# Kernel tuning notes

Measured on AMD Instinct MI355X. Metric: run time of the kernel, lower is better.

The kernel has to match this reference:

```python
import jax, jax.numpy as jnp
import numpy as np

H = 3  # hidden size (matches nn.LSTM(3, 3, ...))


def _lstm_dir(x, Wih, Whh, bih, bhh, reverse):
    """One direction of one LSTM layer. x: [B,T,D]; PyTorch gate order i,f,g,o."""
    B = x.shape[0]
    xT = jnp.swapaxes(x, 0, 1)  # [T,B,D]
    # Precompute input projection for all timesteps (memory-bound GEMM once).
    x_proj = jnp.einsum('tbd,gd->tbg', xT, Wih) + (bih + bhh)  # [T,B,4H]

    def step(carry, xp):
        h, c = carry
        gates = xp + h @ Whh.T  # [B,4H]
        i = jax.nn.sigmoid(gates[:, :H])
        f = jax.nn.sigmoid(gates[:, H:2 * H])
        g = jnp.tanh(gates[:, 2 * H:3 * H])
        o = jax.nn.sigmoid(gates[:, 3 * H:])
        c = f * c + i * g
        h = o * jnp.tanh(c)
        return (h, c), h

    init = (jnp.zeros((B, H), x.dtype), jnp.zeros((B, H), x.dtype))
    _, hs = jax.lax.scan(step, init, x_proj, reverse=reverse)
    return jnp.swapaxes(hs, 0, 1)  # [B,T,H], time-aligned with input


def setup_inputs() -> dict:
    key = jax.random.key(0)
    ks = jax.random.split(key, 20)
    B, T = 8192, 512
    k = 1.0 / np.sqrt(H)

    def u(kk, shape):
        return jax.random.uniform(kk, shape, jnp.float32, -k, k)

    inp = {"x": jax.random.normal(ks[0], (B, T, 3), jnp.float32)}
    # layer 0: input dim 3; layer 1: input dim 2*H = 6
    inp.update({
        "W_ih_l0": u(ks[1], (4 * H, 3)),  "W_hh_l0": u(ks[2], (4 * H, H)),
        "b_ih_l0": u(ks[3], (4 * H,)),    "b_hh_l0": u(ks[4], (4 * H,)),
        "W_ih_l0r": u(ks[5], (4 * H, 3)), "W_hh_l0r": u(ks[6], (4 * H, H)),
        "b_ih_l0r": u(ks[7], (4 * H,)),   "b_hh_l0r": u(ks[8], (4 * H,)),
        "W_ih_l1": u(ks[9], (4 * H, 2 * H)),  "W_hh_l1": u(ks[10], (4 * H, H)),
        "b_ih_l1": u(ks[11], (4 * H,)),       "b_hh_l1": u(ks[12], (4 * H,)),
        "W_ih_l1r": u(ks[13], (4 * H, 2 * H)),"W_hh_l1r": u(ks[14], (4 * H, H)),
        "b_ih_l1r": u(ks[15], (4 * H,)),      "b_hh_l1r": u(ks[16], (4 * H,)),
        "W_lin": u(ks[17], (1, 2 * H)),       "b_lin": u(ks[18], (1,)),
    })
    return inp


def reference(x, W_ih_l0, W_hh_l0, b_ih_l0, b_hh_l0,
              W_ih_l0r, W_hh_l0r, b_ih_l0r, b_hh_l0r,
              W_ih_l1, W_hh_l1, b_ih_l1, b_hh_l1,
              W_ih_l1r, W_hh_l1r, b_ih_l1r, b_hh_l1r,
              W_lin, b_lin):
    # layer 0 (bidirectional)
    y0 = jnp.concatenate([
        _lstm_dir(x, W_ih_l0, W_hh_l0, b_ih_l0, b_hh_l0, False),
        _lstm_dir(x, W_ih_l0r, W_hh_l0r, b_ih_l0r, b_hh_l0r, True),
    ], axis=-1)  # [B,T,6]
    # layer 1 (bidirectional)
    y1 = jnp.concatenate([
        _lstm_dir(y0, W_ih_l1, W_hh_l1, b_ih_l1, b_hh_l1, False),
        _lstm_dir(y0, W_ih_l1r, W_hh_l1r, b_ih_l1r, b_hh_l1r, True),
    ], axis=-1)  # [B,T,6]
    last = y1[:, -1, :]  # [B,6]  (output sequence at final timestep)
    out = last @ W_lin.T + b_lin  # [B,1]
    return jax.nn.sigmoid(out.reshape(-1))  # [B]
```

## Files before the change

kernel.cpp:

```cpp
#include <hip/hip_runtime.h>


#define B_ 8192
#define T_ 512
#define LOG2E 1.4426950408889634f

typedef float v2f __attribute__((ext_vector_type(2)));

__device__ __forceinline__ float rcp_(float x)  { return __builtin_amdgcn_rcpf(x); }
__device__ __forceinline__ float exp2_(float x) { return __builtin_amdgcn_exp2f(x); }
__device__ __forceinline__ float sigm_(float x) {
  return rcp_(1.0f + exp2_(-LOG2E * x));
}
__device__ __forceinline__ float tanh_(float x) {
  return 1.0f - 2.0f * rcp_(1.0f + exp2_(2.0f * LOG2E * x));
}
__device__ __forceinline__ v2f sp(float s) { return (v2f){s, s}; }
__device__ __forceinline__ v2f pkfma(v2f a, float b, v2f c) {
  return __builtin_elementwise_fma(a, sp(b), c);
}

template <int CTRL>
__device__ __forceinline__ float dppf(float v) {
  int s = __float_as_int(v);
  return __int_as_float(__builtin_amdgcn_update_dpp(s, s, CTRL, 0xF, 0xF, false));
}
#define QB0 0x00
#define QB1 0x55
#define QB2 0xAA
#define SHR4 0x114

__global__ __launch_bounds__(256, 1) void lstm_l0_bwd(
    const float* __restrict__ x,
    const float* __restrict__ Wih, const float* __restrict__ Whh,
    const float* __restrict__ bih, const float* __restrict__ bhh,
    float* __restrict__ y0b)
{
  int tid = blockIdx.x * 256 + threadIdx.x;
  int b = tid >> 2, jl = tid & 3;
  int j = (jl < 3) ? jl : 0;
  const int r0 = j, r1 = 3 + j, r2 = 6 + j, r3 = 9 + j;

  v2f wif0 = {Wih[r0*3+0], Wih[r1*3+0]}, wif1 = {Wih[r0*3+1], Wih[r1*3+1]},
      wif2 = {Wih[r0*3+2], Wih[r1*3+2]};
  v2f wif3 = {Whh[r0*3+0], Whh[r1*3+0]}, wif4 = {Whh[r0*3+1], Whh[r1*3+1]},
      wif5 = {Whh[r0*3+2], Whh[r1*3+2]};
  v2f wgo0 = {Wih[r2*3+0], Wih[r3*3+0]}, wgo1 = {Wih[r2*3+1], Wih[r3*3+1]},
      wgo2 = {Wih[r2*3+2], Wih[r3*3+2]};
  v2f wgo3 = {Whh[r2*3+0], Whh[r3*3+0]}, wgo4 = {Whh[r2*3+1], Whh[r3*3+1]},
      wgo5 = {Whh[r2*3+2], Whh[r3*3+2]};
  v2f bif = {bih[r0]+bhh[r0], bih[r1]+bhh[r1]};
  v2f bgo = {bih[r2]+bhh[r2], bih[r3]+bhh[r3]};

  float h = 0.f, c = 0.f, hb0 = 0.f, hb1 = 0.f, hb2 = 0.f;
  const float4* xq = (const float4*)(x + (size_t)b * (T_ * 3));
  float* ywb = y0b + (size_t)b * (T_ * 3) + jl * 8;

  float hs0 = 0.f, hs1 = 0.f, hs2 = 0.f, hs3 = 0.f,
        hs4 = 0.f, hs5 = 0.f, hs6 = 0.f, hs7 = 0.f, h511 = 0.f;
  float4 p0, p1, p2, p3, p4, p5, q0, q1, q2, q3, q4, q5;

#define LD1(blk, r0_, r1_, r2_, r3_, r4_, r5_) do {                       \
    const float4* _p = xq + (blk) * 6;                                    \
    r0_ = _p[0]; r1_ = _p[1]; r2_ = _p[2];                                \
    r3_ = _p[3]; r4_ = _p[4]; r5_ = _p[5];                                \
    __builtin_amdgcn_sched_barrier(0); } while (0)

#define STEP1(x0, x1, x2, HOUT) do {                                      \
    v2f aif = pkfma(wif0, (x0), bif); aif = pkfma(wif1, (x1), aif);       \
    aif = pkfma(wif2, (x2), aif);                                         \
    v2f uif = wif3 * sp(hb0); uif = pkfma(wif4, hb1, uif);                \
    uif = pkfma(wif5, hb2, uif);                                          \
    v2f pif = aif + uif;                                                  \
    v2f ago = pkfma(wgo0, (x0), bgo); ago = pkfma(wgo1, (x1), ago);       \
    ago = pkfma(wgo2, (x2), ago);                                         \
    v2f ugo = wgo3 * sp(hb0); ugo = pkfma(wgo4, hb1, ugo);                \
    ugo = pkfma(wgo5, hb2, ugo);                                          \
    v2f pgo = ago + ugo;                                                  \
    v2f eif = pif * sp(-LOG2E);                                           \
    v2f ego = pgo * (v2f){2.f * LOG2E, -LOG2E};                           \
    float ig = rcp_(1.f + exp2_(eif.x));                                  \
    float fg = rcp_(1.f + exp2_(eif.y));                                  \
    float gg = 1.f - 2.f * rcp_(1.f + exp2_(ego.x));                      \
    float og = rcp_(1.f + exp2_(ego.y));                                  \
    c = fg * c + ig * gg;                                                 \
    h = og * tanh_(c);                                                    \
    hb0 = dppf<QB0>(h); hb1 = dppf<QB1>(h); hb2 = dppf<QB2>(h);           \
    HOUT = h; } while (0)

#define FLUSH1(yblk) do {                                                 \
    if (jl < 3) {                                                         \
      float4* _o = (float4*)(ywb + (yblk) * 24);                          \
      _o[0] = make_float4(hs0, hs1, hs2, hs3);                            \
      _o[1] = make_float4(hs4, hs5, hs6, hs7);                            \
    } } while (0)

#define PROC1(blk, r0_, r1_, r2_, r3_, r4_, r5_, FIRST) do {              \
    STEP1(r5_.y, r5_.z, r5_.w, hs0);                                      \
    if (FIRST) h511 = hs0; else FLUSH1((blk) + 1);                        \
    STEP1(r4_.z, r4_.w, r5_.x, hs7);                                      \
    STEP1(r3_.w, r4_.x, r4_.y, hs6);                                      \
    STEP1(r3_.x, r3_.y, r3_.z, hs5);                                      \
    STEP1(r2_.y, r2_.z, r2_.w, hs4);                                      \
    STEP1(r1_.z, r1_.w, r2_.x, hs3);                                      \
    STEP1(r0_.w, r1_.x, r1_.y, hs2);                                      \
    STEP1(r0_.x, r0_.y, r0_.z, hs1); } while (0)

  LD1(63, p0, p1, p2, p3, p4, p5);
  LD1(62, q0, q1, q2, q3, q4, q5);
  PROC1(63, p0, p1, p2, p3, p4, p5, true);
  LD1(61, p0, p1, p2, p3, p4, p5);
  PROC1(62, q0, q1, q2, q3, q4, q5, false);
  LD1(60, q0, q1, q2, q3, q4, q5);
  for (int blk = 61; blk >= 1; blk -= 2) {
    PROC1(blk, p0, p1, p2, p3, p4, p5, false);
    if (blk >= 3) LD1(blk - 2, p0, p1, p2, p3, p4, p5);
    PROC1(blk - 1, q0, q1, q2, q3, q4, q5, false);
    if (blk >= 3) LD1(blk - 3, q0, q1, q2, q3, q4, q5);
  }
  hs0 = h511;
  FLUSH1(0);
#undef LD1
#undef STEP1
#undef FLUSH1
#undef PROC1
}

__global__ __launch_bounds__(256, 1) void lstm_fused_fwd(
    const float* __restrict__ x,
    const float* __restrict__ Wih0, const float* __restrict__ Whh0,
    const float* __restrict__ bih0, const float* __restrict__ bhh0,
    const float* __restrict__ Wih1, const float* __restrict__ Whh1,
    const float* __restrict__ bih1, const float* __restrict__ bhh1,
    const float* __restrict__ Wih1r, const float* __restrict__ Whh1r,
    const float* __restrict__ bih1r, const float* __restrict__ bhh1r,
    const float* __restrict__ Wlin, const float* __restrict__ blin,
    const float* __restrict__ y0b,
    float* __restrict__ out)
{
  int tid = blockIdx.x * 256 + threadIdx.x;
  int b = tid >> 3, lane = tid & 7;
  bool role1 = lane >= 4;
  int j  = role1 ? (lane - 4) : lane;
  int jc = (j < 3) ? j : 2;
  const int r0 = jc, r1 = 3 + jc, r2 = 6 + jc, r3 = 9 + jc;

  v2f wif0, wif1, wif2, wif3, wif4, wif5, wif6, wif7, wif8;
  v2f wgo0, wgo1, wgo2, wgo3, wgo4, wgo5, wgo6, wgo7, wgo8;
  v2f bif, bgo;
  if (!role1) {
    wif0 = (v2f){Wih0[r0*3+0], Wih0[r1*3+0]};
    wif1 = (v2f){Wih0[r0*3+1], Wih0[r1*3+1]};
    wif2 = (v2f){Wih0[r0*3+2], Wih0[r1*3+2]};
    wif3 = (v2f){0.f, 0.f}; wif4 = (v2f){0.f, 0.f}; wif5 = (v2f){0.f, 0.f};
    wif6 = (v2f){Whh0[r0*3+0], Whh0[r1*3+0]};
    wif7 = (v2f){Whh0[r0*3+1], Whh0[r1*3+1]};
    wif8 = (v2f){Whh0[r0*3+2], Whh0[r1*3+2]};
    wgo0 = (v2f){Wih0[r2*3+0], Wih0[r3*3+0]};
    wgo1 = (v2f){Wih0[r2*3+1], Wih0[r3*3+1]};
    wgo2 = (v2f){Wih0[r2*3+2], Wih0[r3*3+2]};
    wgo3 = (v2f){0.f, 0.f}; wgo4 = (v2f){0.f, 0.f}; wgo5 = (v2f){0.f, 0.f};
    wgo6 = (v2f){Whh0[r2*3+0], Whh0[r3*3+0]};
    wgo7 = (v2f){Whh0[r2*3+1], Whh0[r3*3+1]};
    wgo8 = (v2f){Whh0[r2*3+2], Whh0[r3*3+2]};
    bif = (v2f){bih0[r0]+bhh0[r0], bih0[r1]+bhh0[r1]};
    bgo = (v2f){bih0[r2]+bhh0[r2], bih0[r3]+bhh0[r3]};
  } else {
    wif0 = (v2f){Wih1[r0*6+0], Wih1[r1*6+0]};
    wif1 = (v2f){Wih1[r0*6+1], Wih1[r1*6+1]};
    wif2 = (v2f){Wih1[r0*6+2], Wih1[r1*6+2]};
    wif3 = (v2f){Wih1[r0*6+3], Wih1[r1*6+3]};
    wif4 = (v2f){Wih1[r0*6+4], Wih1[r1*6+4]};
    wif5 = (v2f){Wih1[r0*6+5], Wih1[r1*6+5]};
    wif6 = (v2f){Whh1[r0*3+0], Whh1[r1*3+0]};
    wif7 = (v2f){Whh1[r0*3+1], Whh1[r1*3+1]};
    wif8 = (v2f){Whh1[r0*3+2], Whh1[r1*3+2]};
    wgo0 = (v2f){Wih1[r2*6+0], Wih1[r3*6+0]};
    wgo1 = (v2f){Wih1[r2*6+1], Wih1[r3*6+1]};
    wgo2 = (v2f){Wih1[r2*6+2], Wih1[r3*6+2]};
    wgo3 = (v2f){Wih1[r2*6+3], Wih1[r3*6+3]};
    wgo4 = (v2f){Wih1[r2*6+4], Wih1[r3*6+4]};
    wgo5 = (v2f){Wih1[r2*6+5], Wih1[r3*6+5]};
    wgo6 = (v2f){Whh1[r2*3+0], Whh1[r3*3+0]};
    wgo7 = (v2f){Whh1[r2*3+1], Whh1[r3*3+1]};
    wgo8 = (v2f){Whh1[r2*3+2], Whh1[r3*3+2]};
    bif = (v2f){bih1[r0]+bhh1[r0], bih1[r1]+bhh1[r1]};
    bgo = (v2f){bih1[r2]+bhh1[r2], bih1[r3]+bhh1[r3]};
  }

  float h = 0.f, c = 0.f;
  float ha0 = 0.f, ha1 = 0.f, ha2 = 0.f;
  float hb0 = 0.f, hb1 = 0.f, hb2 = 0.f;
  const float4* baseq =
      (const float4*)((role1 ? y0b : x) + (size_t)b * (T_ * 3));

  const float* up = y0b + (size_t)b * (T_ * 3);
  float ub0 = up[0], ub1 = up[8], ub2 = up[16];

  float4 p0, p1, p2, p3, p4, p5, q0, q1, q2, q3, q4, q5;

#define LD2(blk, r0_, r1_, r2_, r3_, r4_, r5_) do {                       \
    const float4* _p = baseq + (blk) * 6;                                 \
    r0_ = _p[0]; r1_ = _p[1]; r2_ = _p[2];                                \
    r3_ = _p[3]; r4_ = _p[4]; r5_ = _p[5];                                \
    __builtin_amdgcn_sched_barrier(0); } while (0)

#define GATES2(m0, m1, m2, n0, n1, n2)                     \
    float v0 = role1 ? hb0 : (m0);                                        \
    float v1 = role1 ? hb1 : (m1);                                        \
    float v2 = role1 ? hb2 : (m2);                                        \
    v2f aif = pkfma(wif0, v0, bif); aif = pkfma(wif1, v1, aif);           \
    aif = pkfma(wif2, v2, aif);                                           \
    aif = pkfma(wif3, (n0), aif); aif = pkfma(wif4, (n1), aif);           \
    v2f uif = wif5 * sp(n2); uif = pkfma(wif6, ha0, uif);                 \
    uif = pkfma(wif7, ha1, uif); uif = pkfma(wif8, ha2, uif);             \
    v2f pif = aif + uif;                                                  \
    v2f ago = pkfma(wgo0, v0, bgo); ago = pkfma(wgo1, v1, ago);           \
    ago = pkfma(wgo2, v2, ago);                                           \
    ago = pkfma(wgo3, (n0), ago); ago = pkfma(wgo4, (n1), ago);           \
    v2f ugo = wgo5 * sp(n2); ugo = pkfma(wgo6, ha0, ugo);                 \
    ugo = pkfma(wgo7, ha1, ugo); ugo = pkfma(wgo8, ha2, ugo);             \
    v2f pgo = ago + ugo;                                                  \
    v2f eif = pif * sp(-LOG2E);                                           \
    v2f ego = pgo * (v2f){2.f * LOG2E, -LOG2E};                           \
    float ig = rcp_(1.f + exp2_(eif.x));                                  \
    float fg = rcp_(1.f + exp2_(eif.y));                                  \
    float gg = 1.f - 2.f * rcp_(1.f + exp2_(ego.x));                      \
    float og = rcp_(1.f + exp2_(ego.y));                                  \
    float cn = fg * c + ig * gg;                                          \
    float hn = og * tanh_(cn);

#define BCAST2() do {                                                     \
    ha0 = dppf<QB0>(h); ha1 = dppf<QB1>(h); ha2 = dppf<QB2>(h);           \
    hb0 = dppf<SHR4>(ha0); hb1 = dppf<SHR4>(ha1); hb2 = dppf<SHR4>(ha2);  \
  } while (0)

#define STEP2(m0, m1, m2, n0, n1, n2) do {                                \
    GATES2(m0, m1, m2, n0, n1, n2)                                        \
    c = cn; h = hn;                                                       \
    BCAST2(); } while (0)

#define STEP2V(m0, m1, m2, n0, n1, n2, VALID) do {                        \
    GATES2(m0, m1, m2, n0, n1, n2)                                        \
    c = (VALID) ? cn : c; h = (VALID) ? hn : h;                           \
    BCAST2(); } while (0)

#define PROC2(r0_, r1_, r2_, r3_, r4_, r5_) do {                          \
    STEP2(r0_.x, r0_.y, r0_.z,  r0_.x, r2_.x, r4_.x);                     \
    STEP2(r0_.w, r1_.x, r1_.y,  r0_.y, r2_.y, r4_.y);                     \
    STEP2(r1_.z, r1_.w, r2_.x,  r0_.z, r2_.z, r4_.z);                     \
    STEP2(r2_.y, r2_.z, r2_.w,  r0_.w, r2_.w, r4_.w);                     \
    STEP2(r3_.x, r3_.y, r3_.z,  r1_.x, r3_.x, r5_.x);                     \
    STEP2(r3_.w, r4_.x, r4_.y,  r1_.y, r3_.y, r5_.y);                     \
    STEP2(r4_.z, r4_.w, r5_.x,  r1_.z, r3_.z, r5_.z);                     \
    STEP2(r5_.y, r5_.z, r5_.w,  r1_.w, r3_.w, r5_.w); } while (0)

  LD2(0, p0, p1, p2, p3, p4, p5);
  LD2(1, q0, q1, q2, q3, q4, q5);
  STEP2V(p0.x, p0.y, p0.z,  p0.x, p2.x, p4.x, !role1);
  STEP2(p0.w, p1.x, p1.y,  p0.y, p2.y, p4.y);
  STEP2(p1.z, p1.w, p2.x,  p0.z, p2.z, p4.z);
  STEP2(p2.y, p2.z, p2.w,  p0.w, p2.w, p4.w);
  STEP2(p3.x, p3.y, p3.z,  p1.x, p3.x, p5.x);
  STEP2(p3.w, p4.x, p4.y,  p1.y, p3.y, p5.y);
  STEP2(p4.z, p4.w, p5.x,  p1.z, p3.z, p5.z);
  STEP2(p5.y, p5.z, p5.w,  p1.w, p3.w, p5.w);
  LD2(2, p0, p1, p2, p3, p4, p5);
  PROC2(q0, q1, q2, q3, q4, q5);
  LD2(3, q0, q1, q2, q3, q4, q5);
  for (int blk = 2; blk < 64; blk += 2) {
    PROC2(p0, p1, p2, p3, p4, p5);
    if (blk + 2 < 64) LD2(blk + 2, p0, p1, p2, p3, p4, p5);
    PROC2(q0, q1, q2, q3, q4, q5);
    if (blk + 3 < 64) LD2(blk + 3, q0, q1, q2, q3, q4, q5);
  }
  STEP2V(ub0, ub1, ub2,  ub0, ub1, ub2, role1);

  float e0 = role1 ? hb0 : ha0;
  float e1 = role1 ? hb1 : ha1;
  float e2 = role1 ? hb2 : ha2;

  float h1b;
  {
    float q_i = bih1r[r0] + bhh1r[r0]
              + Wih1r[r0*6+0]*e0 + Wih1r[r0*6+1]*e1 + Wih1r[r0*6+2]*e2
              + Wih1r[r0*6+3]*ub0 + Wih1r[r0*6+4]*ub1 + Wih1r[r0*6+5]*ub2;
    float q_g = bih1r[r2] + bhh1r[r2]
              + Wih1r[r2*6+0]*e0 + Wih1r[r2*6+1]*e1 + Wih1r[r2*6+2]*e2
              + Wih1r[r2*6+3]*ub0 + Wih1r[r2*6+4]*ub1 + Wih1r[r2*6+5]*ub2;
    float q_o = bih1r[r3] + bhh1r[r3]
              + Wih1r[r3*6+0]*e0 + Wih1r[r3*6+1]*e1 + Wih1r[r3*6+2]*e2
              + Wih1r[r3*6+3]*ub0 + Wih1r[r3*6+4]*ub1 + Wih1r[r3*6+5]*ub2;
    float ig = sigm_(q_i), gg = tanh_(q_g), og = sigm_(q_o);
    h1b = og * tanh_(ig * gg);
  }

  float part = 0.f;
  if (role1) { if (j < 3) part = Wlin[j]     * h;   }
  else       { if (j < 3) part = Wlin[3 + j] * h1b; }
  part += __shfl_xor(part, 1, 8);
  part += __shfl_xor(part, 2, 8);
  part += __shfl_xor(part, 4, 8);
  if (lane == 0) out[b] = sigm_(part + blin[0]);
#undef LD2
#undef GATES2
#undef BCAST2
#undef STEP2
#undef STEP2V
#undef PROC2
}

extern "C" void kernel_launch(void* const* d_in, const int* in_sizes, int n_in,
                              void* d_out, int out_size, void* d_ws, size_t ws_size,
                              hipStream_t stream) {
  const float* x        = (const float*)d_in[0];
  const float* W_ih_l0  = (const float*)d_in[1];
  const float* W_hh_l0  = (const float*)d_in[2];
  const float* b_ih_l0  = (const float*)d_in[3];
  const float* b_hh_l0  = (const float*)d_in[4];
  const float* W_ih_l0r = (const float*)d_in[5];
  const float* W_hh_l0r = (const float*)d_in[6];
  const float* b_ih_l0r = (const float*)d_in[7];
  const float* b_hh_l0r = (const float*)d_in[8];
  const float* W_ih_l1  = (const float*)d_in[9];
  const float* W_hh_l1  = (const float*)d_in[10];
  const float* b_ih_l1  = (const float*)d_in[11];
  const float* b_hh_l1  = (const float*)d_in[12];
  const float* W_ih_l1r = (const float*)d_in[13];
  const float* W_hh_l1r = (const float*)d_in[14];
  const float* b_ih_l1r = (const float*)d_in[15];
  const float* b_hh_l1r = (const float*)d_in[16];
  const float* W_lin    = (const float*)d_in[17];
  const float* b_lin    = (const float*)d_in[18];

  float* y0b = (float*)d_ws;
  float* out = (float*)d_out;

  lstm_l0_bwd<<<(B_ * 4) / 256, 256, 0, stream>>>(
      x, W_ih_l0r, W_hh_l0r, b_ih_l0r, b_hh_l0r, y0b);

  lstm_fused_fwd<<<(B_ * 8) / 256, 256, 0, stream>>>(
      x, W_ih_l0, W_hh_l0, b_ih_l0, b_hh_l0,
      W_ih_l1, W_hh_l1, b_ih_l1, b_hh_l1,
      W_ih_l1r, W_hh_l1r, b_ih_l1r, b_hh_l1r,
      W_lin, b_lin, y0b, out);
}
```

Baseline: 151.9 us.

## Split gate pairs across lanes to double thread parallelism per LSTM cell

Each hidden unit's four gates were computed by one lane as two packed pairs. They are now split across two lanes: one computes i/f, the other g/o, and the results are exchanged with DPP row shifts. Thread counts double for both kernels, and launch bounds move to two blocks per CU. This halves the per-lane transcendental and FMA work on the serial recurrence chain and adds parallelism, at the cost of extra DPP shuffles and selects per step and more redundant input loads.

```diff
diff --git a/kernel.cpp b/kernel.cpp
--- a/kernel.cpp
+++ b/kernel.cpp
@@ -28,33 +28,34 @@
 #define QB0 0x00
 #define QB1 0x55
 #define QB2 0xAA
+#define SHL4 0x104
 #define SHR4 0x114
-
-__global__ __launch_bounds__(256, 1) void lstm_l0_bwd(
+#define SHR8 0x118
+
+__global__ __launch_bounds__(256, 2) void lstm_l0_bwd(
     const float* __restrict__ x,
     const float* __restrict__ Wih, const float* __restrict__ Whh,
     const float* __restrict__ bih, const float* __restrict__ bhh,
     float* __restrict__ y0b)
 {
   int tid = blockIdx.x * 256 + threadIdx.x;
-  int b = tid >> 2, jl = tid & 3;
-  int j = (jl < 3) ? jl : 0;
-  const int r0 = j, r1 = 3 + j, r2 = 6 + j, r3 = 9 + j;
-
-  v2f wif0 = {Wih[r0*3+0], Wih[r1*3+0]}, wif1 = {Wih[r0*3+1], Wih[r1*3+1]},
-      wif2 = {Wih[r0*3+2], Wih[r1*3+2]};
-  v2f wif3 = {Whh[r0*3+0], Whh[r1*3+0]}, wif4 = {Whh[r0*3+1], Whh[r1*3+1]},
-      wif5 = {Whh[r0*3+2], Whh[r1*3+2]};
-  v2f wgo0 = {Wih[r2*3+0], Wih[r3*3+0]}, wgo1 = {Wih[r2*3+1], Wih[r3*3+1]},
-      wgo2 = {Wih[r2*3+2], Wih[r3*3+2]};
-  v2f wgo3 = {Whh[r2*3+0], Whh[r3*3+0]}, wgo4 = {Whh[r2*3+1], Whh[r3*3+1]},
-      wgo5 = {Whh[r2*3+2], Whh[r3*3+2]};
-  v2f bif = {bih[r0]+bhh[r0], bih[r1]+bhh[r1]};
-  v2f bgo = {bih[r2]+bhh[r2], bih[r3]+bhh[r3]};
-
-  float h = 0.f, c = 0.f, hb0 = 0.f, hb1 = 0.f, hb2 = 0.f;
+  int b = tid >> 3, lane = tid & 7;
+  bool qgo = (lane & 4) != 0;
+  int j = lane & 3; int jj = (j < 3) ? j : 0;
+  const int ra = (qgo ? 6 : 0) + jj, rb = ra + 3;
+
+  v2f w0 = {Wih[ra*3+0], Wih[rb*3+0]}, w1 = {Wih[ra*3+1], Wih[rb*3+1]},
+      w2 = {Wih[ra*3+2], Wih[rb*3+2]};
+  v2f u0 = {Whh[ra*3+0], Whh[rb*3+0]}, u1 = {Whh[ra*3+1], Whh[rb*3+1]},
+      u2 = {Whh[ra*3+2], Whh[rb*3+2]};
+  v2f b2 = {bih[ra]+bhh[ra], bih[rb]+bhh[rb]};
+  v2f sv = qgo ? (v2f){-2.f*LOG2E, -LOG2E} : (v2f){-LOG2E, -LOG2E};
+  v2f av = qgo ? (v2f){2.f, 1.f}  : (v2f){1.f, 1.f};
+  v2f dv = qgo ? (v2f){-1.f, 0.f} : (v2f){0.f, 0.f};
+
+  float h = 0.f, c = 0.f, ha0 = 0.f, ha1 = 0.f, ha2 = 0.f;
   const float4* xq = (const float4*)(x + (size_t)b * (T_ * 3));
-  float* ywb = y0b + (size_t)b * (T_ * 3) + jl * 8;
+  float* ywb = y0b + (size_t)b * (T_ * 3) + jj * 8;
 
   float hs0 = 0.f, hs1 = 0.f, hs2 = 0.f, hs3 = 0.f,
         hs4 = 0.f, hs5 = 0.f, hs6 = 0.f, hs7 = 0.f, h511 = 0.f;
@@ -67,29 +68,29 @@
     __builtin_amdgcn_sched_barrier(0); } while (0)
 
 #define STEP1(x0, x1, x2, HOUT) do {                                      \
-    v2f aif = pkfma(wif0, (x0), bif); aif = pkfma(wif1, (x1), aif);       \
-    aif = pkfma(wif2, (x2), aif);                                         \
-    v2f uif = wif3 * sp(hb0); uif = pkfma(wif4, hb1, uif);                \
-    uif = pkfma(wif5, hb2, uif);                                          \
-    v2f pif = aif + uif;                                                  \
-    v2f ago = pkfma(wgo0, (x0), bgo); ago = pkfma(wgo1, (x1), ago);       \
-    ago = pkfma(wgo2, (x2), ago);                                         \
-    v2f ugo = wgo3 * sp(hb0); ugo = pkfma(wgo4, hb1, ugo);                \
-    ugo = pkfma(wgo5, hb2, ugo);                                          \
-    v2f pgo = ago + ugo;                                                  \
-    v2f eif = pif * sp(-LOG2E);                                           \
-    v2f ego = pgo * (v2f){2.f * LOG2E, -LOG2E};                           \
-    float ig = rcp_(1.f + exp2_(eif.x));                                  \
-    float fg = rcp_(1.f + exp2_(eif.y));                                  \
-    float gg = 1.f - 2.f * rcp_(1.f + exp2_(ego.x));                      \
-    float og = rcp_(1.f + exp2_(ego.y));                                  \
-    c = fg * c + ig * gg;                                                 \
-    h = og * tanh_(c);                                                    \
-    hb0 = dppf<QB0>(h); hb1 = dppf<QB1>(h); hb2 = dppf<QB2>(h);           \
+    v2f pv = pkfma(w0, (x0), b2); pv = pkfma(w1, (x1), pv);               \
+    pv = pkfma(w2, (x2), pv);                                             \
+    v2f uv = u0 * sp(ha0); uv = pkfma(u1, ha1, uv);                       \
+    uv = pkfma(u2, ha2, uv);                                              \
+    pv = pv + uv;                                                         \
+    v2f e = pv * sv;                                                      \
+    float r0v = rcp_(1.f + exp2_(e.x));                                   \
+    float r1v = rcp_(1.f + exp2_(e.y));                                   \
+    float axv = __builtin_fmaf(av.x, r0v, dv.x);                          \
+    float ayv = __builtin_fmaf(av.y, r1v, dv.y);                          \
+    float slx = dppf<SHL4>(axv), sly = dppf<SHL4>(ayv);                   \
+    float srx = dppf<SHR4>(axv), sry = dppf<SHR4>(ayv);                   \
+    float gi = qgo ? srx : axv;                                           \
+    float gf = qgo ? sry : ayv;                                           \
+    float gG = qgo ? axv : slx;                                           \
+    float gO = qgo ? ayv : sly;                                           \
+    c = gf * c + gi * gG;                                                 \
+    h = gO * tanh_(c);                                                    \
+    ha0 = dppf<QB0>(h); ha1 = dppf<QB1>(h); ha2 = dppf<QB2>(h);           \
     HOUT = h; } while (0)
 
 #define FLUSH1(yblk) do {                                                 \
-    if (jl < 3) {                                                         \
+    if (lane < 3) {                                                       \
       float4* _o = (float4*)(ywb + (yblk) * 24);                          \
       _o[0] = make_float4(hs0, hs1, hs2, hs3);                            \
       _o[1] = make_float4(hs4, hs5, hs6, hs7);                            \
@@ -126,7 +127,7 @@
 #undef PROC1
 }
 
-__global__ __launch_bounds__(256, 1) void lstm_fused_fwd(
+__global__ __launch_bounds__(256, 2) void lstm_fused_fwd(
     const float* __restrict__ x,
     const float* __restrict__ Wih0, const float* __restrict__ Whh0,
     const float* __restrict__ bih0, const float* __restrict__ bhh0,
@@ -139,60 +140,43 @@
     float* __restrict__ out)
 {
   int tid = blockIdx.x * 256 + threadIdx.x;
-  int b = tid >> 3, lane = tid & 7;
-  bool role1 = lane >= 4;
-  int j  = role1 ? (lane - 4) : lane;
-  int jc = (j < 3) ? j : 2;
-  const int r0 = jc, r1 = 3 + jc, r2 = 6 + jc, r3 = 9 + jc;
-
-  v2f wif0, wif1, wif2, wif3, wif4, wif5, wif6, wif7, wif8;
-  v2f wgo0, wgo1, wgo2, wgo3, wgo4, wgo5, wgo6, wgo7, wgo8;
-  v2f bif, bgo;
-  if (!role1) {
-    wif0 = (v2f){Wih0[r0*3+0], Wih0[r1*3+0]};
-    wif1 = (v2f){Wih0[r0*3+1], Wih0[r1*3+1]};
-    wif2 = (v2f){Wih0[r0*3+2], Wih0[r1*3+2]};
-    wif3 = (v2f){0.f, 0.f}; wif4 = (v2f){0.f, 0.f}; wif5 = (v2f){0.f, 0.f};
-    wif6 = (v2f){Whh0[r0*3+0], Whh0[r1*3+0]};
-    wif7 = (v2f){Whh0[r0*3+1], Whh0[r1*3+1]};
-    wif8 = (v2f){Whh0[r0*3+2], Whh0[r1*3+2]};
-    wgo0 = (v2f){Wih0[r2*3+0], Wih0[r3*3+0]};
-    wgo1 = (v2f){Wih0[r2*3+1], Wih0[r3*3+1]};
-    wgo2 = (v2f){Wih0[r2*3+2], Wih0[r3*3+2]};
-    wgo3 = (v2f){0.f, 0.f}; wgo4 = (v2f){0.f, 0.f}; wgo5 = (v2f){0.f, 0.f};
-    wgo6 = (v2f){Whh0[r2*3+0], Whh0[r3*3+0]};
-    wgo7 = (v2f){Whh0[r2*3+1], Whh0[r3*3+1]};
-    wgo8 = (v2f){Whh0[r2*3+2], Whh0[r3*3+2]};
-    bif = (v2f){bih0[r0]+bhh0[r0], bih0[r1]+bhh0[r1]};
-    bgo = (v2f){bih0[r2]+bhh0[r2], bih0[r3]+bhh0[r3]};
+  int b = tid >> 4, lane = tid & 15;
+  bool cell1 = lane >= 8;
+  bool qgo = (lane & 4) != 0;
+  int j = lane & 3; int jj = (j < 3) ? j : 0;
+  const int ra = (qgo ? 6 : 0) + jj, rb = ra + 3;
+
+  v2f w0, w1, w2, w3, w4, w5, u0, u1, u2, b2;
+  if (!cell1) {
+    w0 = (v2f){Wih0[ra*3+0], Wih0[rb*3+0]};
+    w1 = (v2f){Wih0[ra*3+1], Wih0[rb*3+1]};
+    w2 = (v2f){Wih0[ra*3+2], Wih0[rb*3+2]};
+    w3 = (v2f){0.f, 0.f}; w4 = (v2f){0.f, 0.f}; w5 = (v2f){0.f, 0.f};
+    u0 = (v2f){Whh0[ra*3+0], Whh0[rb*3+0]};
+    u1 = (v2f){Whh0[ra*3+1], Whh0[rb*3+1]};
+    u2 = (v2f){Whh0[ra*3+2], Whh0[rb*3+2]};
+    b2 = (v2f){bih0[ra]+bhh0[ra], bih0[rb]+bhh0[rb]};
   } else {
-    wif0 = (v2f){Wih1[r0*6+0], Wih1[r1*6+0]};
-    wif1 = (v2f){Wih1[r0*6+1], Wih1[r1*6+1]};
-    wif2 = (v2f){Wih1[r0*6+2], Wih1[r1*6+2]};
-    wif3 = (v2f){Wih1[r0*6+3], Wih1[r1*6+3]};
-    wif4 = (v2f){Wih1[r0*6+4], Wih1[r1*6+4]};
-    wif5 = (v2f){Wih1[r0*6+5], Wih1[r1*6+5]};
-    wif6 = (v2f){Whh1[r0*3+0], Whh1[r1*3+0]};
-    wif7 = (v2f){Whh1[r0*3+1], Whh1[r1*3+1]};
-    wif8 = (v2f){Whh1[r0*3+2], Whh1[r1*3+2]};
-    wgo0 = (v2f){Wih1[r2*6+0], Wih1[r3*6+0]};
-    wgo1 = (v2f){Wih1[r2*6+1], Wih1[r3*6+1]};
-    wgo2 = (v2f){Wih1[r2*6+2], Wih1[r3*6+2]};
-    wgo3 = (v2f){Wih1[r2*6+3], Wih1[r3*6+3]};
-    wgo4 = (v2f){Wih1[r2*6+4], Wih1[r3*6+4]};
-    wgo5 = (v2f){Wih1[r2*6+5], Wih1[r3*6+5]};
-    wgo6 = (v2f){Whh1[r2*3+0], Whh1[r3*3+0]};
-    wgo7 = (v2f){Whh1[r2*3+1], Whh1[r3*3+1]};
-    wgo8 = (v2f){Whh1[r2*3+2], Whh1[r3*3+2]};
-    bif = (v2f){bih1[r0]+bhh1[r0], bih1[r1]+bhh1[r1]};
-    bgo = (v2f){bih1[r2]+bhh1[r2], bih1[r3]+bhh1[r3]};
+    w0 = (v2f){Wih1[ra*6+0], Wih1[rb*6+0]};
+    w1 = (v2f){Wih1[ra*6+1], Wih1[rb*6+1]};
+    w2 = (v2f){Wih1[ra*6+2], Wih1[rb*6+2]};
+    w3 = (v2f){Wih1[ra*6+3], Wih1[rb*6+3]};
+    w4 = (v2f){Wih1[ra*6+4], Wih1[rb*6+4]};
+    w5 = (v2f){Wih1[ra*6+5], Wih1[rb*6+5]};
+    u0 = (v2f){Whh1[ra*3+0], Whh1[rb*3+0]};
+    u1 = (v2f){Whh1[ra*3+1], Whh1[rb*3+1]};
+    u2 = (v2f){Whh1[ra*3+2], Whh1[rb*3+2]};
+    b2 = (v2f){bih1[ra]+bhh1[ra], bih1[rb]+bhh1[rb]};
   }
+  v2f sv = qgo ? (v2f){-2.f*LOG2E, -LOG2E} : (v2f){-LOG2E, -LOG2E};
+  v2f av = qgo ? (v2f){2.f, 1.f}  : (v2f){1.f, 1.f};
+  v2f dv = qgo ? (v2f){-1.f, 0.f} : (v2f){0.f, 0.f};
 
   float h = 0.f, c = 0.f;
   float ha0 = 0.f, ha1 = 0.f, ha2 = 0.f;
   float hb0 = 0.f, hb1 = 0.f, hb2 = 0.f;
   const float4* baseq =
-      (const float4*)((role1 ? y0b : x) + (size_t)b * (T_ * 3));
+      (const float4*)((cell1 ? y0b : x) + (size_t)b * (T_ * 3));
 
   const float* up = y0b + (size_t)b * (T_ * 3);
   float ub0 = up[0], ub1 = up[8], ub2 = up[16];
@@ -206,33 +190,32 @@
     __builtin_amdgcn_sched_barrier(0); } while (0)
 
 #define GATES2(m0, m1, m2, n0, n1, n2)                     \
-    float v0 = role1 ? hb0 : (m0);                                        \
-    float v1 = role1 ? hb1 : (m1);                                        \
-    float v2 = role1 ? hb2 : (m2);                                        \
-    v2f aif = pkfma(wif0, v0, bif); aif = pkfma(wif1, v1, aif);           \
-    aif = pkfma(wif2, v2, aif);                                           \
-    aif = pkfma(wif3, (n0), aif); aif = pkfma(wif4, (n1), aif);           \
-    v2f uif = wif5 * sp(n2); uif = pkfma(wif6, ha0, uif);                 \
-    uif = pkfma(wif7, ha1, uif); uif = pkfma(wif8, ha2, uif);             \
-    v2f pif = aif + uif;                                                  \
-    v2f ago = pkfma(wgo0, v0, bgo); ago = pkfma(wgo1, v1, ago);           \
-    ago = pkfma(wgo2, v2, ago);                                           \
-    ago = pkfma(wgo3, (n0), ago); ago = pkfma(wgo4, (n1), ago);           \
-    v2f ugo = wgo5 * sp(n2); ugo = pkfma(wgo6, ha0, ugo);                 \
-    ugo = pkfma(wgo7, ha1, ugo); ugo = pkfma(wgo8, ha2, ugo);             \
-    v2f pgo = ago + ugo;                                                  \
-    v2f eif = pif * sp(-LOG2E);                                           \
-    v2f ego = pgo * (v2f){2.f * LOG2E, -LOG2E};                           \
-    float ig = rcp_(1.f + exp2_(eif.x));                                  \
-    float fg = rcp_(1.f + exp2_(eif.y));                                  \
-    float gg = 1.f - 2.f * rcp_(1.f + exp2_(ego.x));                      \
-    float og = rcp_(1.f + exp2_(ego.y));                                  \
-    float cn = fg * c + ig * gg;                                          \
-    float hn = og * tanh_(cn);
+    float i0 = cell1 ? hb0 : (m0);                                        \
+    float i1 = cell1 ? hb1 : (m1);                                        \
+    float i2 = cell1 ? hb2 : (m2);                                        \
+    v2f pv = pkfma(w0, i0, b2); pv = pkfma(w1, i1, pv);                   \
+    pv = pkfma(w2, i2, pv);                                               \
+    pv = pkfma(w3, (n0), pv); pv = pkfma(w4, (n1), pv);                   \
+    v2f uv = w5 * sp(n2); uv = pkfma(u0, ha0, uv);                        \
+    uv = pkfma(u1, ha1, uv); uv = pkfma(u2, ha2, uv);                     \
+    pv = pv + uv;                                                         \
+    v2f e = pv * sv;                                                      \
+    float r0v = rcp_(1.f + exp2_(e.x));                                   \
+    float r1v = rcp_(1.f + exp2_(e.y));                                   \
+    float axv = __builtin_fmaf(av.x, r0v, dv.x);                          \
+    float ayv = __builtin_fmaf(av.y, r1v, dv.y);                          \
+    float slx = dppf<SHL4>(axv), sly = dppf<SHL4>(ayv);                   \
+    float srx = dppf<SHR4>(axv), sry = dppf<SHR4>(ayv);                   \
+    float gi = qgo ? srx : axv;                                           \
+    float gf = qgo ? sry : ayv;                                           \
+    float gG = qgo ? axv : slx;                                           \
+    float gO = qgo ? ayv : sly;                                           \
+    float cn = gf * c + gi * gG;                                          \
+    float hn = gO * tanh_(cn);
 
 #define BCAST2() do {                                                     \
     ha0 = dppf<QB0>(h); ha1 = dppf<QB1>(h); ha2 = dppf<QB2>(h);           \
-    hb0 = dppf<SHR4>(ha0); hb1 = dppf<SHR4>(ha1); hb2 = dppf<SHR4>(ha2);  \
+    hb0 = dppf<SHR8>(ha0); hb1 = dppf<SHR8>(ha1); hb2 = dppf<SHR8>(ha2);  \
   } while (0)
 
 #define STEP2(m0, m1, m2, n0, n1, n2) do {                                \
@@ -257,7 +240,7 @@
 
   LD2(0, p0, p1, p2, p3, p4, p5);
   LD2(1, q0, q1, q2, q3, q4, q5);
-  STEP2V(p0.x, p0.y, p0.z,  p0.x, p2.x, p4.x, !role1);
+  STEP2V(p0.x, p0.y, p0.z,  p0.x, p2.x, p4.x, !cell1);
   STEP2(p0.w, p1.x, p1.y,  p0.y, p2.y, p4.y);
   STEP2(p1.z, p1.w, p2.x,  p0.z, p2.z, p4.z);
   STEP2(p2.y, p2.z, p2.w,  p0.w, p2.w, p4.w);
@@ -274,33 +257,45 @@
     PROC2(q0, q1, q2, q3, q4, q5);
     if (blk + 3 < 64) LD2(blk + 3, q0, q1, q2, q3, q4, q5);
   }
-  STEP2V(ub0, ub1, ub2,  ub0, ub1, ub2, role1);
-
-  float e0 = role1 ? hb0 : ha0;
-  float e1 = role1 ? hb1 : ha1;
-  float e2 = role1 ? hb2 : ha2;
+  STEP2V(ub0, ub1, ub2,  ub0, ub1, ub2, cell1);
+
+  float e0 = cell1 ? hb0 : ha0;
+  float e1 = cell1 ? hb1 : ha1;
+  float e2 = cell1 ? hb2 : ha2;
 
   float h1b;
   {
-    float q_i = bih1r[r0] + bhh1r[r0]
-              + Wih1r[r0*6+0]*e0 + Wih1r[r0*6+1]*e1 + Wih1r[r0*6+2]*e2
-              + Wih1r[r0*6+3]*ub0 + Wih1r[r0*6+4]*ub1 + Wih1r[r0*6+5]*ub2;
-    float q_g = bih1r[r2] + bhh1r[r2]
-              + Wih1r[r2*6+0]*e0 + Wih1r[r2*6+1]*e1 + Wih1r[r2*6+2]*e2
-              + Wih1r[r2*6+3]*ub0 + Wih1r[r2*6+4]*ub1 + Wih1r[r2*6+5]*ub2;
-    float q_o = bih1r[r3] + bhh1r[r3]
-              + Wih1r[r3*6+0]*e0 + Wih1r[r3*6+1]*e1 + Wih1r[r3*6+2]*e2
-              + Wih1r[r3*6+3]*ub0 + Wih1r[r3*6+4]*ub1 + Wih1r[r3*6+5]*ub2;
-    float ig = sigm_(q_i), gg = tanh_(q_g), og = sigm_(q_o);
-    h1b = og * tanh_(ig * gg);
+    v2f x0w = {Wih1r[ra*6+0], Wih1r[rb*6+0]};
+    v2f x1w = {Wih1r[ra*6+1], Wih1r[rb*6+1]};
+    v2f x2w = {Wih1r[ra*6+2], Wih1r[rb*6+2]};
+    v2f x3w = {Wih1r[ra*6+3], Wih1r[rb*6+3]};
+    v2f x4w = {Wih1r[ra*6+4], Wih1r[rb*6+4]};
+    v2f x5w = {Wih1r[ra*6+5], Wih1r[rb*6+5]};
+    v2f brv = {bih1r[ra]+bhh1r[ra], bih1r[rb]+bhh1r[rb]};
+    v2f pv = pkfma(x0w, e0, brv); pv = pkfma(x1w, e1, pv);
+    pv = pkfma(x2w, e2, pv);      pv = pkfma(x3w, ub0, pv);
+    pv = pkfma(x4w, ub1, pv);     pv = pkfma(x5w, ub2, pv);
+    v2f e = pv * sv;
+    float r0v = rcp_(1.f + exp2_(e.x));
+    float r1v = rcp_(1.f + exp2_(e.y));
+    float axv = __builtin_fmaf(av.x, r0v, dv.x);
+    float ayv = __builtin_fmaf(av.y, r1v, dv.y);
+    float slx = dppf<SHL4>(axv);
+    float sly = dppf<SHL4>(ayv);
+    float srx = dppf<SHR4>(axv);
+    float gi = qgo ? srx : axv;
+    float gG = qgo ? axv : slx;
+    float gO = qgo ? ayv : sly;
+    float cb = gi * gG;
+    h1b = gO * tanh_(cb);
   }
 
   float part = 0.f;
-  if (role1) { if (j < 3) part = Wlin[j]     * h;   }
-  else       { if (j < 3) part = Wlin[3 + j] * h1b; }
-  part += __shfl_xor(part, 1, 8);
-  part += __shfl_xor(part, 2, 8);
-  part += __shfl_xor(part, 4, 8);
+  if (!qgo && j < 3) part = cell1 ? (Wlin[j] * h) : (Wlin[3 + j] * h1b);
+  part += __shfl_xor(part, 1, 16);
+  part += __shfl_xor(part, 2, 16);
+  part += __shfl_xor(part, 4, 16);
+  part += __shfl_xor(part, 8, 16);
   if (lane == 0) out[b] = sigm_(part + blin[0]);
 #undef LD2
 #undef GATES2
@@ -336,10 +331,10 @@
   float* y0b = (float*)d_ws;
   float* out = (float*)d_out;
 
-  lstm_l0_bwd<<<(B_ * 4) / 256, 256, 0, stream>>>(
+  lstm_l0_bwd<<<(B_ * 8) / 256, 256, 0, stream>>>(
       x, W_ih_l0r, W_hh_l0r, b_ih_l0r, b_hh_l0r, y0b);
 
-  lstm_fused_fwd<<<(B_ * 8) / 256, 256, 0, stream>>>(
+  lstm_fused_fwd<<<(B_ * 16) / 256, 256, 0, stream>>>(
       x, W_ih_l0, W_hh_l0, b_ih_l0, b_hh_l0,
       W_ih_l1, W_hh_l1, b_ih_l1, b_hh_l1,
       W_ih_l1r, W_hh_l1r, b_ih_l1r, b_hh_l1r,
```

Result: slower. 189.9 us (+25.1%).

## Split backward layer-0 gates across 8 lanes and pre-scale weights by log2e

Applied to the files above, without the earlier changes.

The backward layer-0 kernel now uses 8 lanes per batch row instead of 4. Each half computes two gates (i/f or g/o), and partial products are exchanged with DPP row shifts, which halves the per-lane gate arithmetic on the serial recurrence. Weights and biases in both kernels are pre-multiplied by -log2e (or -2log2e for g) so the exp2 arguments need no extra scaling per step. The fused kernel also splits the accumulation chains into shorter parallel sums. The cost is twice as many threads and extra DPP and select instructions in each step.

```diff
diff --git a/kernel.cpp b/kernel.cpp
--- a/kernel.cpp
+++ b/kernel.cpp
@@ -15,6 +15,8 @@
 __device__ __forceinline__ float tanh_(float x) {
   return 1.0f - 2.0f * rcp_(1.0f + exp2_(2.0f * LOG2E * x));
 }
+__device__ __forceinline__ float act_(float p) { return rcp_(1.f + exp2_(p)); }
+
 __device__ __forceinline__ v2f sp(float s) { return (v2f){s, s}; }
 __device__ __forceinline__ v2f pkfma(v2f a, float b, v2f c) {
   return __builtin_elementwise_fma(a, sp(b), c);
@@ -28,6 +30,7 @@
 #define QB0 0x00
 #define QB1 0x55
 #define QB2 0xAA
+#define SHL4 0x104
 #define SHR4 0x114
 
 __global__ __launch_bounds__(256, 1) void lstm_l0_bwd(
@@ -37,24 +40,26 @@
     float* __restrict__ y0b)
 {
   int tid = blockIdx.x * 256 + threadIdx.x;
-  int b = tid >> 2, jl = tid & 3;
-  int j = (jl < 3) ? jl : 0;
-  const int r0 = j, r1 = 3 + j, r2 = 6 + j, r3 = 9 + j;
-
-  v2f wif0 = {Wih[r0*3+0], Wih[r1*3+0]}, wif1 = {Wih[r0*3+1], Wih[r1*3+1]},
-      wif2 = {Wih[r0*3+2], Wih[r1*3+2]};
-  v2f wif3 = {Whh[r0*3+0], Whh[r1*3+0]}, wif4 = {Whh[r0*3+1], Whh[r1*3+1]},
-      wif5 = {Whh[r0*3+2], Whh[r1*3+2]};
-  v2f wgo0 = {Wih[r2*3+0], Wih[r3*3+0]}, wgo1 = {Wih[r2*3+1], Wih[r3*3+1]},
-      wgo2 = {Wih[r2*3+2], Wih[r3*3+2]};
-  v2f wgo3 = {Whh[r2*3+0], Whh[r3*3+0]}, wgo4 = {Whh[r2*3+1], Whh[r3*3+1]},
-      wgo5 = {Whh[r2*3+2], Whh[r3*3+2]};
-  v2f bif = {bih[r0]+bhh[r0], bih[r1]+bhh[r1]};
-  v2f bgo = {bih[r2]+bhh[r2], bih[r3]+bhh[r3]};
-
-  float h = 0.f, c = 0.f, hb0 = 0.f, hb1 = 0.f, hb2 = 0.f;
+  int b = tid >> 3, lane = tid & 7;
+  bool qgo = (lane & 4) != 0;
+  int j = lane & 3; int jj = (j < 3) ? j : 0;
+  const int ra = (qgo ? 6 : 0) + jj, rb = ra + 3;
+  const float kx = qgo ? (-2.f * LOG2E) : (-LOG2E);
+  const float ky = -LOG2E;
+
+  v2f w0 = {Wih[ra*3+0]*kx, Wih[rb*3+0]*ky},
+      w1 = {Wih[ra*3+1]*kx, Wih[rb*3+1]*ky},
+      w2 = {Wih[ra*3+2]*kx, Wih[rb*3+2]*ky};
+  v2f u0 = {Whh[ra*3+0]*kx, Whh[rb*3+0]*ky},
+      u1 = {Whh[ra*3+1]*kx, Whh[rb*3+1]*ky},
+      u2 = {Whh[ra*3+2]*kx, Whh[rb*3+2]*ky};
+  v2f b2 = {(bih[ra]+bhh[ra])*kx, (bih[rb]+bhh[rb])*ky};
+  const float avx = qgo ? 2.f : 1.f;
+  const float dvx = qgo ? -1.f : 0.f;
+
+  float h = 0.f, c = 0.f, ha0 = 0.f, ha1 = 0.f, ha2 = 0.f;
   const float4* xq = (const float4*)(x + (size_t)b * (T_ * 3));
-  float* ywb = y0b + (size_t)b * (T_ * 3) + jl * 8;
+  float* ywb = y0b + (size_t)b * (T_ * 3) + jj * 8;
 
   float hs0 = 0.f, hs1 = 0.f, hs2 = 0.f, hs3 = 0.f,
         hs4 = 0.f, hs5 = 0.f, hs6 = 0.f, hs7 = 0.f, h511 = 0.f;
@@ -67,29 +72,28 @@
     __builtin_amdgcn_sched_barrier(0); } while (0)
 
 #define STEP1(x0, x1, x2, HOUT) do {                                      \
-    v2f aif = pkfma(wif0, (x0), bif); aif = pkfma(wif1, (x1), aif);       \
-    aif = pkfma(wif2, (x2), aif);                                         \
-    v2f uif = wif3 * sp(hb0); uif = pkfma(wif4, hb1, uif);                \
-    uif = pkfma(wif5, hb2, uif);                                          \
-    v2f pif = aif + uif;                                                  \
-    v2f ago = pkfma(wgo0, (x0), bgo); ago = pkfma(wgo1, (x1), ago);       \
-    ago = pkfma(wgo2, (x2), ago);                                         \
-    v2f ugo = wgo3 * sp(hb0); ugo = pkfma(wgo4, hb1, ugo);                \
-    ugo = pkfma(wgo5, hb2, ugo);                                          \
-    v2f pgo = ago + ugo;                                                  \
-    v2f eif = pif * sp(-LOG2E);                                           \
-    v2f ego = pgo * (v2f){2.f * LOG2E, -LOG2E};                           \
-    float ig = rcp_(1.f + exp2_(eif.x));                                  \
-    float fg = rcp_(1.f + exp2_(eif.y));                                  \
-    float gg = 1.f - 2.f * rcp_(1.f + exp2_(ego.x));                      \
-    float og = rcp_(1.f + exp2_(ego.y));                                  \
-    c = fg * c + ig * gg;                                                 \
-    h = og * tanh_(c);                                                    \
-    hb0 = dppf<QB0>(h); hb1 = dppf<QB1>(h); hb2 = dppf<QB2>(h);           \
+    v2f pv = pkfma(w0, (x0), b2); pv = pkfma(w1, (x1), pv);               \
+    pv = pkfma(w2, (x2), pv);                                             \
+    v2f uv = u0 * sp(ha0); uv = pkfma(u1, ha1, uv);                       \
+    uv = pkfma(u2, ha2, uv);                                              \
+    pv = pv + uv;                                                         \
+    float r0v = act_(pv.x);                                               \
+    float ayv = act_(pv.y);                         \
+    float axv = __builtin_fmaf(avx, r0v, dvx);  \
+    float slx = dppf<SHL4>(axv), sly = dppf<SHL4>(ayv);                   \
+    float srx = dppf<SHR4>(axv), sry = dppf<SHR4>(ayv);                   \
+    float pig = axv * (qgo ? srx : slx);           \
+    float gf  = qgo ? sry : ayv;                                          \
+    float gO  = qgo ? ayv : sly;                                          \
+    c = __builtin_fmaf(gf, c, pig);                                       \
+    float th = __builtin_fmaf(                                            \
+        2.f, rcp_(1.f + exp2_(-2.f * LOG2E * c)), -1.f);                  \
+    h = gO * th;                                                          \
+    ha0 = dppf<QB0>(h); ha1 = dppf<QB1>(h); ha2 = dppf<QB2>(h);           \
     HOUT = h; } while (0)
 
 #define FLUSH1(yblk) do {                                                 \
-    if (jl < 3) {                                                         \
+    if (lane < 3) {                                                       \
       float4* _o = (float4*)(ywb + (yblk) * 24);                          \
       _o[0] = make_float4(hs0, hs1, hs2, hs3);                            \
       _o[1] = make_float4(hs4, hs5, hs6, hs7);                            \
@@ -144,48 +148,49 @@
   int j  = role1 ? (lane - 4) : lane;
   int jc = (j < 3) ? j : 2;
   const int r0 = jc, r1 = 3 + jc, r2 = 6 + jc, r3 = 9 + jc;
+  const float sI = -LOG2E, sG = -2.f * LOG2E;
 
   v2f wif0, wif1, wif2, wif3, wif4, wif5, wif6, wif7, wif8;
   v2f wgo0, wgo1, wgo2, wgo3, wgo4, wgo5, wgo6, wgo7, wgo8;
   v2f bif, bgo;
   if (!role1) {
-    wif0 = (v2f){Wih0[r0*3+0], Wih0[r1*3+0]};
-    wif1 = (v2f){Wih0[r0*3+1], Wih0[r1*3+1]};
-    wif2 = (v2f){Wih0[r0*3+2], Wih0[r1*3+2]};
+    wif0 = (v2f){Wih0[r0*3+0]*sI, Wih0[r1*3+0]*sI};
+    wif1 = (v2f){Wih0[r0*3+1]*sI, Wih0[r1*3+1]*sI};
+    wif2 = (v2f){Wih0[r0*3+2]*sI, Wih0[r1*3+2]*sI};
     wif3 = (v2f){0.f, 0.f}; wif4 = (v2f){0.f, 0.f}; wif5 = (v2f){0.f, 0.f};
-    wif6 = (v2f){Whh0[r0*3+0], Whh0[r1*3+0]};
-    wif7 = (v2f){Whh0[r0*3+1], Whh0[r1*3+1]};
-    wif8 = (v2f){Whh0[r0*3+2], Whh0[r1*3+2]};
-    wgo0 = (v2f){Wih0[r2*3+0], Wih0[r3*3+0]};
-    wgo1 = (v2f){Wih0[r2*3+1], Wih0[r3*3+1]};
-    wgo2 = (v2f){Wih0[r2*3+2], Wih0[r3*3+2]};
+    wif6 = (v2f){Whh0[r0*3+0]*sI, Whh0[r1*3+0]*sI};
+    wif7 = (v2f){Whh0[r0*3+1]*sI, Whh0[r1*3+1]*sI};
+    wif8 = (v2f){Whh0[r0*3+2]*sI, Whh0[r1*3+2]*sI};
+    wgo0 = (v2f){Wih0[r2*3+0]*sG, Wih0[r3*3+0]*sI};
+    wgo1 = (v2f){Wih0[r2*3+1]*sG, Wih0[r3*3+1]*sI};
+    wgo2 = (v2f){Wih0[r2*3+2]*sG, Wih0[r3*3+2]*sI};
     wgo3 = (v2f){0.f, 0.f}; wgo4 = (v2f){0.f, 0.f}; wgo5 = (v2f){0.f, 0.f};
-    wgo6 = (v2f){Whh0[r2*3+0], Whh0[r3*3+0]};
-    wgo7 = (v2f){Whh0[r2*3+1], Whh0[r3*3+1]};
-    wgo8 = (v2f){Whh0[r2*3+2], Whh0[r3*3+2]};
-    bif = (v2f){bih0[r0]+bhh0[r0], bih0[r1]+bhh0[r1]};
-    bgo = (v2f){bih0[r2]+bhh0[r2], bih0[r3]+bhh0[r3]};
+    wgo6 = (v2f){Whh0[r2*3+0]*sG, Whh0[r3*3+0]*sI};
+    wgo7 = (v2f){Whh0[r2*3+1]*sG, Whh0[r3*3+1]*sI};
+    wgo8 = (v2f){Whh0[r2*3+2]*sG, Whh0[r3*3+2]*sI};
+    bif = (v2f){(bih0[r0]+bhh0[r0])*sI, (bih0[r1]+bhh0[r1])*sI};
+    bgo = (v2f){(bih0[r2]+bhh0[r2])*sG, (bih0[r3]+bhh0[r3])*sI};
   } else {
-    wif0 = (v2f){Wih1[r0*6+0], Wih1[r1*6+0]};
-    wif1 = (v2f){Wih1[r0*6+1], Wih1[r1*6+1]};
-    wif2 = (v2f){Wih1[r0*6+2], Wih1[r1*6+2]};
-    wif3 = (v2f){Wih1[r0*6+3], Wih1[r1*6+3]};
-    wif4 = (v2f){Wih1[r0*6+4], Wih1[r1*6+4]};
-    wif5 = (v2f){Wih1[r0*6+5], Wih1[r1*6+5]};
-    wif6 = (v2f){Whh1[r0*3+0], Whh1[r1*3+0]};
-    wif7 = (v2f){Whh1[r0*3+1], Whh1[r1*3+1]};
-    wif8 = (v2f){Whh1[r0*3+2], Whh1[r1*3+2]};
-    wgo0 = (v2f){Wih1[r2*6+0], Wih1[r3*6+0]};
-    wgo1 = (v2f){Wih1[r2*6+1], Wih1[r3*6+1]};
-    wgo2 = (v2f){Wih1[r2*6+2], Wih1[r3*6+2]};
-    wgo3 = (v2f){Wih1[r2*6+3], Wih1[r3*6+3]};
-    wgo4 = (v2f){Wih1[r2*6+4], Wih1[r3*6+4]};
-    wgo5 = (v2f){Wih1[r2*6+5], Wih1[r3*6+5]};
-    wgo6 = (v2f){Whh1[r2*3+0], Whh1[r3*3+0]};
-    wgo7 = (v2f){Whh1[r2*3+1], Whh1[r3*3+1]};
-    wgo8 = (v2f){Whh1[r2*3+2], Whh1[r3*3+2]};
-    bif = (v2f){bih1[r0]+bhh1[r0], bih1[r1]+bhh1[r1]};
-    bgo = (v2f){bih1[r2]+bhh1[r2], bih1[r3]+bhh1[r3]};
+    wif0 = (v2f){Wih1[r0*6+0]*sI, Wih1[r1*6+0]*sI};
+    wif1 = (v2f){Wih1[r0*6+1]*sI, Wih1[r1*6+1]*sI};
+    wif2 = (v2f){Wih1[r0*6+2]*sI, Wih1[r1*6+2]*sI};
+    wif3 = (v2f){Wih1[r0*6+3]*sI, Wih1[r1*6+3]*sI};
+    wif4 = (v2f){Wih1[r0*6+4]*sI, Wih1[r1*6+4]*sI};
+    wif5 = (v2f){Wih1[r0*6+5]*sI, Wih1[r1*6+5]*sI};
+    wif6 = (v2f){Whh1[r0*3+0]*sI, Whh1[r1*3+0]*sI};
+    wif7 = (v2f){Whh1[r0*3+1]*sI, Whh1[r1*3+1]*sI};
+    wif8 = (v2f){Whh1[r0*3+2]*sI, Whh1[r1*3+2]*sI};
+    wgo0 = (v2f){Wih1[r2*6+0]*sG, Wih1[r3*6+0]*sI};
+    wgo1 = (v2f){Wih1[r2*6+1]*sG, Wih1[r3*6+1]*sI};
+    wgo2 = (v2f){Wih1[r2*6+2]*sG, Wih1[r3*6+2]*sI};
+    wgo3 = (v2f){Wih1[r2*6+3]*sG, Wih1[r3*6+3]*sI};
+    wgo4 = (v2f){Wih1[r2*6+4]*sG, Wih1[r3*6+4]*sI};
+    wgo5 = (v2f){Wih1[r2*6+5]*sG, Wih1[r3*6+5]*sI};
+    wgo6 = (v2f){Whh1[r2*3+0]*sG, Whh1[r3*3+0]*sI};
+    wgo7 = (v2f){Whh1[r2*3+1]*sG, Whh1[r3*3+1]*sI};
+    wgo8 = (v2f){Whh1[r2*3+2]*sG, Whh1[r3*3+2]*sI};
+    bif = (v2f){(bih1[r0]+bhh1[r0])*sI, (bih1[r1]+bhh1[r1])*sI};
+    bgo = (v2f){(bih1[r2]+bhh1[r2])*sG, (bih1[r3]+bhh1[r3])*sI};
   }
 
   float h = 0.f, c = 0.f;
@@ -211,24 +216,26 @@
     float v2 = role1 ? hb2 : (m2);                                        \
     v2f aif = pkfma(wif0, v0, bif); aif = pkfma(wif1, v1, aif);           \
     aif = pkfma(wif2, v2, aif);                                           \
-    aif = pkfma(wif3, (n0), aif); aif = pkfma(wif4, (n1), aif);           \
-    v2f uif = wif5 * sp(n2); uif = pkfma(wif6, ha0, uif);                 \
-    uif = pkfma(wif7, ha1, uif); uif = pkfma(wif8, ha2, uif);             \
-    v2f pif = aif + uif;                                                  \
+    v2f nif = wif3 * sp(n0); nif = pkfma(wif4, (n1), nif);                \
+    nif = pkfma(wif5, (n2), nif);                                         \
+    v2f uif = wif6 * sp(ha0); uif = pkfma(wif7, ha1, uif);                \
+    uif = pkfma(wif8, ha2, uif);                                          \
+    v2f pif = (aif + nif) + uif;                                          \
     v2f ago = pkfma(wgo0, v0, bgo); ago = pkfma(wgo1, v1, ago);           \
     ago = pkfma(wgo2, v2, ago);                                           \
-    ago = pkfma(wgo3, (n0), ago); ago = pkfma(wgo4, (n1), ago);           \
-    v2f ugo = wgo5 * sp(n2); ugo = pkfma(wgo6, ha0, ugo);                 \
-    ugo = pkfma(wgo7, ha1, ugo); ugo = pkfma(wgo8, ha2, ugo);             \
-    v2f pgo = ago + ugo;                                                  \
-    v2f eif = pif * sp(-LOG2E);                                           \
-    v2f ego = pgo * (v2f){2.f * LOG2E, -LOG2E};                           \
-    float ig = rcp_(1.f + exp2_(eif.x));                                  \
-    float fg = rcp_(1.f + exp2_(eif.y));                                  \
-    float gg = 1.f - 2.f * rcp_(1.f + exp2_(ego.x));                      \
-    float og = rcp_(1.f + exp2_(ego.y));                                  \
-    float cn = fg * c + ig * gg;                                          \
-    float hn = og * tanh_(cn);
+    v2f ngo = wgo3 * sp(n0); ngo = pkfma(wgo4, (n1), ngo);                \
+    ngo = pkfma(wgo5, (n2), ngo);                                         \
+    v2f ugo = wgo6 * sp(ha0); ugo = pkfma(wgo7, ha1, ugo);                \
+    ugo = pkfma(wgo8, ha2, ugo);                                          \
+    v2f pgo = (ago + ngo) + ugo;                                          \
+    float ig = act_(pif.x);                                               \
+    float fg = act_(pif.y);                                               \
+    float gg = __builtin_fmaf(2.f, act_(pgo.x), -1.f);                    \
+    float og = act_(pgo.y);                                               \
+    float cn = __builtin_fmaf(fg, c, ig * gg);                            \
+    float th = __builtin_fmaf(                                            \
+        2.f, rcp_(1.f + exp2_(-2.f * LOG2E * cn)), -1.f);                 \
+    float hn = og * th;
 
 #define BCAST2() do {                                                     \
     ha0 = dppf<QB0>(h); ha1 = dppf<QB1>(h); ha2 = dppf<QB2>(h);           \
@@ -336,7 +343,7 @@
   float* y0b = (float*)d_ws;
   float* out = (float*)d_out;
 
-  lstm_l0_bwd<<<(B_ * 4) / 256, 256, 0, stream>>>(
+  lstm_l0_bwd<<<(B_ * 8) / 256, 256, 0, stream>>>(
       x, W_ih_l0r, W_hh_l0r, b_ih_l0r, b_hh_l0r, y0b);
 
   lstm_fused_fwd<<<(B_ * 8) / 256, 256, 0, stream>>>(
```

Result: faster. 142.6 us (-6.1%).
